# Kernel optimization log

Hardware: AMD Instinct MI355X
Metric: run time of the kernel (lower is better)

## Reference

```python
import jax, jax.numpy as jnp
import numpy as np

B, N, IN, H, DK, DV, OUT = 8, 1024, 512, 8, 64, 64, 512
SCALE = 1.0 / (DK ** 0.5)


def setup_inputs() -> dict:
    key = jax.random.key(0)
    ks = jax.random.split(key, 10)
    s = lambda fan_in: 1.0 / np.sqrt(fan_in)
    return {
        "x": jax.random.normal(ks[0], (B, N, IN), dtype=jnp.float32),
        "Wv": jax.random.uniform(ks[1], (IN, H * DV), jnp.float32, -s(IN), s(IN)),
        "bv": jax.random.uniform(ks[2], (H * DV,), jnp.float32, -s(IN), s(IN)),
        "Wk": jax.random.uniform(ks[3], (IN, H * DK), jnp.float32, -s(IN), s(IN)),
        "bk": jax.random.uniform(ks[4], (H * DK,), jnp.float32, -s(IN), s(IN)),
        "Wq": jax.random.uniform(ks[5], (IN, H * DK), jnp.float32, -s(IN), s(IN)),
        "bq": jax.random.uniform(ks[6], (H * DK,), jnp.float32, -s(IN), s(IN)),
        "Wo": jax.random.uniform(ks[7], (H * DV, OUT), jnp.float32, -s(H * DV), s(H * DV)),
        "bo": jax.random.uniform(ks[8], (OUT,), jnp.float32, -s(H * DV), s(H * DV)),
        "mask": jax.random.randint(ks[9], (B, N, N), 0, 2, dtype=jnp.int32),
    }


def reference(x, Wv, bv, Wk, bk, Wq, bq, Wo, bo, mask):
    # projections -> (B, N, H, d), vkq activation = relu
    v = jax.nn.relu((x @ Wv + bv).reshape(B, N, H, DV))
    q = jax.nn.relu((x @ Wq + bq).reshape(B, N, H, DK))
    k = jax.nn.relu((x @ Wk + bk).reshape(B, N, H, DK))
    # (B, H, N, d)
    q, k, v = (t.transpose(0, 2, 1, 3) for t in (q, k, v))
    # raw attention weights (returned pre-mask, pre-softmax): (B, H, N, N)
    att_weights = jnp.einsum("bhqd,bhkd->bhqk", q, k) * SCALE
    att = jnp.where(mask[:, None, :, :] == 0, -1e9, att_weights)
    att = jax.nn.softmax(att, axis=-1)
    out = jnp.einsum("bhqk,bhkd->bhqd", att, v) + v  # residual add of v
    out = out.transpose(0, 2, 1, 3).reshape(B, N, H * DV)
    out = jax.nn.relu(out @ Wo + bo)  # final activation = relu
    return out, att_weights
```

## Files before the change

kernel.cpp:

```cpp
#include <hip/hip_runtime.h>
#include <hip/hip_bf16.h>

typedef __attribute__((ext_vector_type(8))) short short8;
typedef __attribute__((ext_vector_type(4))) float f32x4;

#define DEV static __device__ __forceinline__

DEV unsigned short f2bf(float f) {
  union { float f; unsigned u; } v; v.f = f;
  unsigned r = v.u + 0x7FFFu + ((v.u >> 16) & 1u);
  return (unsigned short)(r >> 16);
}
DEV float bf2f(unsigned short b) {
  union { unsigned u; float f; } v; v.u = ((unsigned)b) << 16;
  return v.f;
}

DEV unsigned cvtpk_bf16(float lo, float hi) {
  unsigned r;
  asm("v_cvt_pk_bf16_f32 %0, %1, %2" : "=v"(r) : "v"(lo), "v"(hi));
  return r;
}

DEV void gld_lds16(const void* g, void* l) {
  __builtin_amdgcn_global_load_lds(
      (const __attribute__((address_space(1))) unsigned int*)g,
      (__attribute__((address_space(3))) unsigned int*)l, 16, 0, 0);
}

DEV short8 lds_read8(const unsigned short* base, int byteoff) {
  return *reinterpret_cast<const short8*>(reinterpret_cast<const char*>(base) + byteoff);
}

__global__ __launch_bounds__(256) void cast_x_kernel(const float* __restrict__ x,
                                                     unsigned short* __restrict__ xb, int n4) {
  int i = blockIdx.x * blockDim.x + threadIdx.x;
  if (i >= n4) return;
  float4 v = reinterpret_cast<const float4*>(x)[i];
  ushort4 o;
  o.x = f2bf(v.x); o.y = f2bf(v.y); o.z = f2bf(v.z); o.w = f2bf(v.w);
  reinterpret_cast<ushort4*>(xb)[i] = o;
}

__global__ __launch_bounds__(256) void mask_prep_kernel(const int* __restrict__ mask,
                                                        unsigned char* __restrict__ mb) {
  int i = blockIdx.x * 256 + threadIdx.x;
  int bq = i >> 8;
  int q = bq & 1023;
  int k = (i & 255) * 4;
  int4 m4 = reinterpret_cast<const int4*>(mask)[i];
  unsigned v = (m4.x ? 1u : 0u) | ((m4.y ? 1u : 0u) << 8) |
               ((m4.z ? 1u : 0u) << 16) | ((m4.w ? 1u : 0u) << 24);
  *reinterpret_cast<unsigned*>(mb + (size_t)bq * 1024 + (k ^ ((q & 7) << 2))) = v;
}

__global__ __launch_bounds__(256) void transpose_w_kernel(
    const float* __restrict__ W0, const float* __restrict__ W1,
    const float* __restrict__ W2, const float* __restrict__ W3,
    unsigned short* __restrict__ T0, unsigned short* __restrict__ T1,
    unsigned short* __restrict__ T2, unsigned short* __restrict__ T3) {
  const float* W = blockIdx.z == 0 ? W0 : blockIdx.z == 1 ? W1 : blockIdx.z == 2 ? W2 : W3;
  unsigned short* T = blockIdx.z == 0 ? T0 : blockIdx.z == 1 ? T1 : blockIdx.z == 2 ? T2 : T3;
  __shared__ unsigned short tile[32][33];
  int tx = threadIdx.x & 31, ty = threadIdx.x >> 5;
  int n0 = blockIdx.x * 32, k0 = blockIdx.y * 32;
#pragma unroll
  for (int i = 0; i < 32; i += 8)
    tile[ty + i][tx] = f2bf(W[(size_t)(k0 + ty + i) * 512 + n0 + tx]);
  __syncthreads();
#pragma unroll
  for (int i = 0; i < 32; i += 8)
    T[(size_t)(n0 + ty + i) * 512 + k0 + tx] = tile[tx][ty + i];
}

__global__ __launch_bounds__(256) void gemm_proj_kernel(
    const unsigned short* __restrict__ xb,
    const unsigned short* __restrict__ WqT, const unsigned short* __restrict__ WkT,
    const unsigned short* __restrict__ WvT,
    const float* __restrict__ bq, const float* __restrict__ bk, const float* __restrict__ bv,
    unsigned short* __restrict__ qn, unsigned short* __restrict__ kn,
    unsigned short* __restrict__ vn, unsigned short* __restrict__ vT) {
  const int z = blockIdx.z;
  const unsigned short* Wt = z == 0 ? WqT : z == 1 ? WkT : WvT;
  const float* bias = z == 0 ? bq : z == 1 ? bk : bv;
  unsigned short* outp = z == 0 ? qn : z == 1 ? kn : vn;

  __shared__ unsigned short smem[17408];
  unsigned short* As = smem;
  unsigned short* Bs = smem + 4096;

  const int tid = threadIdx.x;
  const int lane = tid & 63;
  const int w = tid >> 6;
  const int wm = w >> 1, wn = w & 1;
  const int lr = lane & 15;
  const int g = lane >> 4;

  const int m0 = blockIdx.x * 128;
  const int n0 = blockIdx.y * 128;

  f32x4 acc[4][4];
#pragma unroll
  for (int i = 0; i < 4; ++i)
#pragma unroll
    for (int j = 0; j < 4; ++j) acc[i][j] = (f32x4){0.f, 0.f, 0.f, 0.f};

  for (int kt = 0; kt < 16; ++kt) {
    const int k0 = kt * 32;
    __syncthreads();
#pragma unroll
    for (int p = 0; p < 2; ++p) {
      int slot = tid + 256 * p;
      int r = slot >> 2;
      int kg = (slot & 3) ^ ((r >> 1) & 3);
      unsigned short* ldsA = As + (size_t)((tid >> 6) + 4 * p) * 512;
      unsigned short* ldsB = Bs + (size_t)((tid >> 6) + 4 * p) * 512;
      gld_lds16(xb + (size_t)(m0 + r) * 512 + k0 + kg * 8, ldsA);
      gld_lds16(Wt + (size_t)(n0 + r) * 512 + k0 + kg * 8, ldsB);
    }
    __syncthreads();
    short8 af[4], bfr[4];
#pragma unroll
    for (int mi = 0; mi < 4; ++mi) {
      int r = wm * 64 + mi * 16 + lr;
      af[mi] = lds_read8(As, (r * 64 + g * 16) ^ (((r >> 1) & 3) << 4));
    }
#pragma unroll
    for (int ni = 0; ni < 4; ++ni) {
      int r = wn * 64 + ni * 16 + lr;
      bfr[ni] = lds_read8(Bs, (r * 64 + g * 16) ^ (((r >> 1) & 3) << 4));
    }
#pragma unroll
    for (int mi = 0; mi < 4; ++mi)
#pragma unroll
      for (int ni = 0; ni < 4; ++ni)
        acc[mi][ni] = __builtin_amdgcn_mfma_f32_16x16x32_bf16(af[mi], bfr[ni], acc[mi][ni], 0, 0, 0);
  }
  __syncthreads();

  float biasv[4];
#pragma unroll
  for (int ni = 0; ni < 4; ++ni) biasv[ni] = bias[n0 + wn * 64 + ni * 16 + lr];

#pragma unroll
  for (int mi = 0; mi < 4; ++mi) {
    int rowb = m0 + wm * 64 + mi * 16 + g * 4;
#pragma unroll
    for (int ni = 0; ni < 4; ++ni) {
      int c = n0 + wn * 64 + ni * 16 + lr;
      int h = c >> 6, d = c & 63;
#pragma unroll
      for (int rr = 0; rr < 4; ++rr) {
        float vf = acc[mi][ni][rr] + biasv[ni];
        vf = vf > 0.f ? vf : 0.f;
        unsigned short bvv = f2bf(vf);
        int row = rowb + rr;
        int b = row >> 10, tok = row & 1023;
        outp[((size_t)(b * 8 + h) * 1024 + tok) * 64 + d] = bvv;
        if (z == 2) {
          int cl = wn * 64 + ni * 16 + lr;
          int rl = wm * 64 + mi * 16 + g * 4 + rr;
          smem[cl * 136 + rl] = bvv;
        }
      }
    }
  }
  if (z == 2) {
    __syncthreads();
    int cl = tid >> 1, half = tid & 1;
    int gc = n0 + cl, h = gc >> 6, d = gc & 63;
    int b = m0 >> 10;
    int tokbase = (m0 & 1023) + half * 64;
    size_t base = (size_t)(b * 8 + h) * 65536 + (size_t)d * 1024 + tokbase;
    const unsigned short* src = smem + cl * 136 + half * 64;
#pragma unroll
    for (int j = 0; j < 8; ++j) {
      short8 v8 = *reinterpret_cast<const short8*>(src + j * 8);
      *reinterpret_cast<short8*>(vT + base + j * 8) = v8;
    }
  }
}

__global__ __launch_bounds__(256) void attn_kernel(
    const unsigned short* __restrict__ qg, const unsigned short* __restrict__ kgp,
    const unsigned short* __restrict__ vg, const unsigned short* __restrict__ vTg,
    const unsigned char* __restrict__ mb, float* __restrict__ attw,
    unsigned short* __restrict__ Og) {
  __shared__ unsigned short Ks[4096];
  __shared__ unsigned short Vs[4096];
  __shared__ unsigned char Mb[4096];
  __shared__ unsigned short Ps[4096];

  const int tid = threadIdx.x, lane = tid & 63, w = tid >> 6;
  const int lr = lane & 15, g = lane >> 4;
  const int bh = blockIdx.y, b = bh >> 3, h = bh & 7;
  const int q0 = blockIdx.x * 64;
  const int qw = q0 + w * 16;
  const size_t qbase = (size_t)bh * 65536;

  short8 aq[2];
#pragma unroll
  for (int dc = 0; dc < 2; ++dc)
    aq[dc] = *reinterpret_cast<const short8*>(qg + qbase + (size_t)(qw + lr) * 64 + dc * 32 + g * 8);

  f32x4 o[4];
#pragma unroll
  for (int di = 0; di < 4; ++di) o[di] = (f32x4){0.f, 0.f, 0.f, 0.f};
  float lsum = 0.f;

  unsigned short* Pw = Ps + w * 1024;
  const int gq = qw + lr;
  const int mrow = w * 16 + lr;

  for (int t = 0; t < 16; ++t) {
    const int kv0 = t * 64;
    __syncthreads();
#pragma unroll
    for (int p = 0; p < 2; ++p) {
      int slot = tid + 256 * p;
      int r = slot >> 3;
      int kgx = (slot & 7) ^ (r & 7);
      gld_lds16(kgp + qbase + (size_t)(kv0 + r) * 64 + kgx * 8,
                reinterpret_cast<char*>(Ks) + (w + 4 * p) * 1024);
      gld_lds16(vTg + qbase + (size_t)r * 1024 + kv0 + kgx * 8,
                reinterpret_cast<char*>(Vs) + (w + 4 * p) * 1024);
    }
    {
      int r = tid >> 2, seg = tid & 3;
      gld_lds16(mb + (size_t)(b * 1024 + q0 + r) * 1024 + kv0 + seg * 16,
                reinterpret_cast<char*>(Mb) + w * 1024);
    }
    __syncthreads();

    f32x4 s[4];
#pragma unroll
    for (int ni = 0; ni < 4; ++ni) s[ni] = (f32x4){0.f, 0.f, 0.f, 0.f};
#pragma unroll
    for (int ni = 0; ni < 4; ++ni) {
      int row = ni * 16 + lr;
#pragma unroll
      for (int dc = 0; dc < 2; ++dc) {
        short8 ak = lds_read8(Ks, (row * 128 + dc * 64 + g * 16) ^ ((row & 7) << 4));
        s[ni] = __builtin_amdgcn_mfma_f32_16x16x32_bf16(ak, aq[dc], s[ni], 0, 0, 0);
      }
    }

#pragma unroll
    for (int ni = 0; ni < 4; ++ni) {
      f32x4 sv = s[ni] * 0.125f;
      *reinterpret_cast<f32x4*>(attw + ((size_t)bh * 1024 + gq) * 1024 + kv0 + ni * 16 + g * 4) = sv;
      unsigned mk = *reinterpret_cast<const unsigned*>(
          Mb + ((mrow * 64 + ni * 16 + g * 4) ^ ((mrow & 7) << 2)));
      float p0 = (mk & 0x000000FFu) ? __expf(sv[0] - 16.f) : 0.f;
      float p1 = (mk & 0x0000FF00u) ? __expf(sv[1] - 16.f) : 0.f;
      float p2 = (mk & 0x00FF0000u) ? __expf(sv[2] - 16.f) : 0.f;
      float p3 = (mk & 0xFF000000u) ? __expf(sv[3] - 16.f) : 0.f;
      lsum += (p0 + p1) + (p2 + p3);
      uint2 pk = make_uint2(cvtpk_bf16(p0, p1), cvtpk_bf16(p2, p3));
      int pbyte = (lr * 128 + ni * 32 + g * 8) ^ ((lr & 7) << 4);
      *reinterpret_cast<uint2*>(reinterpret_cast<char*>(Pw) + pbyte) = pk;
    }

#pragma unroll
    for (int kc = 0; kc < 2; ++kc) {
      short8 ap = lds_read8(Pw, (lr * 128 + kc * 64 + g * 16) ^ ((lr & 7) << 4));
#pragma unroll
      for (int di = 0; di < 4; ++di) {
        int rd = di * 16 + lr;
        short8 bv8 = lds_read8(Vs, (rd * 128 + kc * 64 + g * 16) ^ ((rd & 7) << 4));
        o[di] = __builtin_amdgcn_mfma_f32_16x16x32_bf16(ap, bv8, o[di], 0, 0, 0);
      }
    }
  }

  float l = lsum;
  l += __shfl_xor(l, 16);
  l += __shfl_xor(l, 32);

#pragma unroll
  for (int rr = 0; rr < 4; ++rr) {
    int gq2 = qw + g * 4 + rr;
    float lq = __shfl(l, g * 4 + rr);
    float inv = 1.f / lq;
#pragma unroll
    for (int di = 0; di < 4; ++di) {
      int gd = di * 16 + lr;
      float ov = o[di][rr] * inv + bf2f(vg[qbase + (size_t)gq2 * 64 + gd]);
      Og[((size_t)(b * 1024 + gq2)) * 512 + h * 64 + gd] = f2bf(ov);
    }
  }
}

__global__ __launch_bounds__(256) void gemm_out_kernel(
    const unsigned short* __restrict__ Ab, const unsigned short* __restrict__ WoT,
    const float* __restrict__ bo, float* __restrict__ outp) {
  __shared__ unsigned short smem[8192];
  unsigned short* As = smem;
  unsigned short* Bs = smem + 4096;

  const int tid = threadIdx.x;
  const int lane = tid & 63;
  const int w = tid >> 6;
  const int wm = w >> 1, wn = w & 1;
  const int lr = lane & 15;
  const int g = lane >> 4;
  const int m0 = blockIdx.x * 128;
  const int n0 = blockIdx.y * 128;

  f32x4 acc[4][4];
#pragma unroll
  for (int i = 0; i < 4; ++i)
#pragma unroll
    for (int j = 0; j < 4; ++j) acc[i][j] = (f32x4){0.f, 0.f, 0.f, 0.f};

  for (int kt = 0; kt < 16; ++kt) {
    const int k0 = kt * 32;
    __syncthreads();
#pragma unroll
    for (int p = 0; p < 2; ++p) {
      int slot = tid + 256 * p;
      int r = slot >> 2;
      int kg = (slot & 3) ^ ((r >> 1) & 3);
      unsigned short* ldsA = As + (size_t)((tid >> 6) + 4 * p) * 512;
      unsigned short* ldsB = Bs + (size_t)((tid >> 6) + 4 * p) * 512;
      gld_lds16(Ab + (size_t)(m0 + r) * 512 + k0 + kg * 8, ldsA);
      gld_lds16(WoT + (size_t)(n0 + r) * 512 + k0 + kg * 8, ldsB);
    }
    __syncthreads();
    short8 af[4], bfr[4];
#pragma unroll
    for (int mi = 0; mi < 4; ++mi) {
      int r = wm * 64 + mi * 16 + lr;
      af[mi] = lds_read8(As, (r * 64 + g * 16) ^ (((r >> 1) & 3) << 4));
    }
#pragma unroll
    for (int ni = 0; ni < 4; ++ni) {
      int r = wn * 64 + ni * 16 + lr;
      bfr[ni] = lds_read8(Bs, (r * 64 + g * 16) ^ (((r >> 1) & 3) << 4));
    }
#pragma unroll
    for (int mi = 0; mi < 4; ++mi)
#pragma unroll
      for (int ni = 0; ni < 4; ++ni)
        acc[mi][ni] = __builtin_amdgcn_mfma_f32_16x16x32_bf16(af[mi], bfr[ni], acc[mi][ni], 0, 0, 0);
  }

  float biasv[4];
#pragma unroll
  for (int ni = 0; ni < 4; ++ni) biasv[ni] = bo[n0 + wn * 64 + ni * 16 + lr];
#pragma unroll
  for (int mi = 0; mi < 4; ++mi) {
    int rowb = m0 + wm * 64 + mi * 16 + g * 4;
#pragma unroll
    for (int ni = 0; ni < 4; ++ni) {
      int c = n0 + wn * 64 + ni * 16 + lr;
#pragma unroll
      for (int rr = 0; rr < 4; ++rr) {
        float vf = acc[mi][ni][rr] + biasv[ni];
        outp[(size_t)(rowb + rr) * 512 + c] = vf > 0.f ? vf : 0.f;
      }
    }
  }
}

extern "C" void kernel_launch(void* const* d_in, const int* in_sizes, int n_in,
                              void* d_out, int out_size, void* d_ws, size_t ws_size,
                              hipStream_t stream) {
  const float* x = (const float*)d_in[0];
  const float* Wv = (const float*)d_in[1];
  const float* bv = (const float*)d_in[2];
  const float* Wk = (const float*)d_in[3];
  const float* bk = (const float*)d_in[4];
  const float* Wq = (const float*)d_in[5];
  const float* bq = (const float*)d_in[6];
  const float* Wo = (const float*)d_in[7];
  const float* bo = (const float*)d_in[8];
  const int* mask = (const int*)d_in[9];

  char* ws = (char*)d_ws;
  unsigned short* xb  = (unsigned short*)(ws);
  unsigned char*  mbb = (unsigned char*)(ws);
  unsigned short* WqT = (unsigned short*)(ws + 8388608);
  unsigned short* WkT = (unsigned short*)(ws + 8912896);
  unsigned short* WvT = (unsigned short*)(ws + 9437184);
  unsigned short* WoT = (unsigned short*)(ws + 9961472);
  unsigned short* qn  = (unsigned short*)(ws + 10485760);
  unsigned short* kn  = (unsigned short*)(ws + 18874368);
  unsigned short* vn  = (unsigned short*)(ws + 27262976);
  unsigned short* vT  = (unsigned short*)(ws + 35651584);
  unsigned short* Og  = (unsigned short*)(ws + 44040192);

  float* outp = (float*)d_out;
  float* attw = (float*)d_out + 4194304;

  cast_x_kernel<<<4096, 256, 0, stream>>>(x, xb, 1048576);

  dim3 tg(16, 16, 4);
  transpose_w_kernel<<<tg, 256, 0, stream>>>(Wq, Wk, Wv, Wo, WqT, WkT, WvT, WoT);

  dim3 gp(64, 4, 3);
  gemm_proj_kernel<<<gp, 256, 0, stream>>>(xb, WqT, WkT, WvT, bq, bk, bv, qn, kn, vn, vT);

  mask_prep_kernel<<<8192, 256, 0, stream>>>(mask, mbb);

  dim3 ga(16, 64);
  attn_kernel<<<ga, 256, 0, stream>>>(qn, kn, vn, vT, mbb, attw, Og);

  dim3 go(64, 4);
  gemm_out_kernel<<<go, 256, 0, stream>>>(Og, WoT, bo, outp);
}
```

Before: 153.1 us.

## Load K, V and mask tiles directly from global into registers in attention

The attention kernel no longer stages K, V^T and mask tiles through shared memory with block-wide barriers. Each wave now loads its MFMA operands and mask words straight from global memory into registers (L2/L1 shared across the 4 waves), and the mask prep kernel writes a plain unswizzled byte layout to match. This removes both __syncthreads per tile and the LDS traffic, but each wave issues its own redundant global loads of K and V and uses more registers.

```diff
diff --git a/kernel.cpp b/kernel.cpp
--- a/kernel.cpp
+++ b/kernel.cpp
@@ -45,13 +45,10 @@
 __global__ __launch_bounds__(256) void mask_prep_kernel(const int* __restrict__ mask,
                                                         unsigned char* __restrict__ mb) {
   int i = blockIdx.x * 256 + threadIdx.x;
-  int bq = i >> 8;
-  int q = bq & 1023;
-  int k = (i & 255) * 4;
   int4 m4 = reinterpret_cast<const int4*>(mask)[i];
   unsigned v = (m4.x ? 1u : 0u) | ((m4.y ? 1u : 0u) << 8) |
                ((m4.z ? 1u : 0u) << 16) | ((m4.w ? 1u : 0u) << 24);
-  *reinterpret_cast<unsigned*>(mb + (size_t)bq * 1024 + (k ^ ((q & 7) << 2))) = v;
+  reinterpret_cast<unsigned*>(mb)[i] = v;
 }
 
 __global__ __launch_bounds__(256) void transpose_w_kernel(
@@ -186,22 +183,19 @@
     const unsigned short* __restrict__ vg, const unsigned short* __restrict__ vTg,
     const unsigned char* __restrict__ mb, float* __restrict__ attw,
     unsigned short* __restrict__ Og) {
-  __shared__ unsigned short Ks[4096];
-  __shared__ unsigned short Vs[4096];
-  __shared__ unsigned char Mb[4096];
   __shared__ unsigned short Ps[4096];
 
   const int tid = threadIdx.x, lane = tid & 63, w = tid >> 6;
   const int lr = lane & 15, g = lane >> 4;
   const int bh = blockIdx.y, b = bh >> 3, h = bh & 7;
-  const int q0 = blockIdx.x * 64;
-  const int qw = q0 + w * 16;
+  const int qw = blockIdx.x * 64 + w * 16;
   const size_t qbase = (size_t)bh * 65536;
+  const int gq = qw + lr;
 
   short8 aq[2];
 #pragma unroll
   for (int dc = 0; dc < 2; ++dc)
-    aq[dc] = *reinterpret_cast<const short8*>(qg + qbase + (size_t)(qw + lr) * 64 + dc * 32 + g * 8);
+    aq[dc] = *reinterpret_cast<const short8*>(qg + qbase + (size_t)gq * 64 + dc * 32 + g * 8);
 
   f32x4 o[4];
 #pragma unroll
@@ -209,52 +203,49 @@
   float lsum = 0.f;
 
   unsigned short* Pw = Ps + w * 1024;
-  const int gq = qw + lr;
-  const int mrow = w * 16 + lr;
+  const unsigned short* kp = kgp + qbase + (size_t)lr * 64 + g * 8;
+  const unsigned short* vp = vTg + qbase + (size_t)lr * 1024 + g * 8;
+  const unsigned char* mp = mb + ((size_t)(b * 1024 + gq)) * 1024 + g * 4;
+  float* awp = attw + ((size_t)bh * 1024 + gq) * 1024 + g * 4;
 
   for (int t = 0; t < 16; ++t) {
     const int kv0 = t * 64;
-    __syncthreads();
-#pragma unroll
-    for (int p = 0; p < 2; ++p) {
-      int slot = tid + 256 * p;
-      int r = slot >> 3;
-      int kgx = (slot & 7) ^ (r & 7);
-      gld_lds16(kgp + qbase + (size_t)(kv0 + r) * 64 + kgx * 8,
-                reinterpret_cast<char*>(Ks) + (w + 4 * p) * 1024);
-      gld_lds16(vTg + qbase + (size_t)r * 1024 + kv0 + kgx * 8,
-                reinterpret_cast<char*>(Vs) + (w + 4 * p) * 1024);
-    }
-    {
-      int r = tid >> 2, seg = tid & 3;
-      gld_lds16(mb + (size_t)(b * 1024 + q0 + r) * 1024 + kv0 + seg * 16,
-                reinterpret_cast<char*>(Mb) + w * 1024);
-    }
-    __syncthreads();
+
+    short8 ak[4][2], vv[4][2];
+    unsigned mk[4];
+#pragma unroll
+    for (int ni = 0; ni < 4; ++ni)
+#pragma unroll
+      for (int dc = 0; dc < 2; ++dc)
+        ak[ni][dc] =
+            *reinterpret_cast<const short8*>(kp + (size_t)(kv0 + ni * 16) * 64 + dc * 32);
+#pragma unroll
+    for (int di = 0; di < 4; ++di)
+#pragma unroll
+      for (int kc = 0; kc < 2; ++kc)
+        vv[di][kc] =
+            *reinterpret_cast<const short8*>(vp + (size_t)(di * 16) * 1024 + kv0 + kc * 32);
+#pragma unroll
+    for (int ni = 0; ni < 4; ++ni)
+      mk[ni] = *reinterpret_cast<const unsigned*>(mp + kv0 + ni * 16);
 
     f32x4 s[4];
 #pragma unroll
-    for (int ni = 0; ni < 4; ++ni) s[ni] = (f32x4){0.f, 0.f, 0.f, 0.f};
-#pragma unroll
-    for (int ni = 0; ni < 4; ++ni) {
-      int row = ni * 16 + lr;
-#pragma unroll
-      for (int dc = 0; dc < 2; ++dc) {
-        short8 ak = lds_read8(Ks, (row * 128 + dc * 64 + g * 16) ^ ((row & 7) << 4));
-        s[ni] = __builtin_amdgcn_mfma_f32_16x16x32_bf16(ak, aq[dc], s[ni], 0, 0, 0);
-      }
+    for (int ni = 0; ni < 4; ++ni) {
+      s[ni] = (f32x4){0.f, 0.f, 0.f, 0.f};
+      s[ni] = __builtin_amdgcn_mfma_f32_16x16x32_bf16(ak[ni][0], aq[0], s[ni], 0, 0, 0);
+      s[ni] = __builtin_amdgcn_mfma_f32_16x16x32_bf16(ak[ni][1], aq[1], s[ni], 0, 0, 0);
     }
 
 #pragma unroll
     for (int ni = 0; ni < 4; ++ni) {
       f32x4 sv = s[ni] * 0.125f;
-      *reinterpret_cast<f32x4*>(attw + ((size_t)bh * 1024 + gq) * 1024 + kv0 + ni * 16 + g * 4) = sv;
-      unsigned mk = *reinterpret_cast<const unsigned*>(
-          Mb + ((mrow * 64 + ni * 16 + g * 4) ^ ((mrow & 7) << 2)));
-      float p0 = (mk & 0x000000FFu) ? __expf(sv[0] - 16.f) : 0.f;
-      float p1 = (mk & 0x0000FF00u) ? __expf(sv[1] - 16.f) : 0.f;
-      float p2 = (mk & 0x00FF0000u) ? __expf(sv[2] - 16.f) : 0.f;
-      float p3 = (mk & 0xFF000000u) ? __expf(sv[3] - 16.f) : 0.f;
+      *reinterpret_cast<f32x4*>(awp + kv0 + ni * 16) = sv;
+      unsigned m = mk[ni];
+      float p0 = (m & 0x000000FFu) ? __expf(sv[0] - 16.f) : 0.f;
+      float p1 = (m & 0x0000FF00u) ? __expf(sv[1] - 16.f) : 0.f;
+      float p2 = (m & 0x00FF0000u) ? __expf(sv[2] - 16.f) : 0.f;
+      float p3 = (m & 0xFF000000u) ? __expf(sv[3] - 16.f) : 0.f;
       lsum += (p0 + p1) + (p2 + p3);
       uint2 pk = make_uint2(cvtpk_bf16(p0, p1), cvtpk_bf16(p2, p3));
       int pbyte = (lr * 128 + ni * 32 + g * 8) ^ ((lr & 7) << 4);
@@ -265,11 +256,8 @@
     for (int kc = 0; kc < 2; ++kc) {
       short8 ap = lds_read8(Pw, (lr * 128 + kc * 64 + g * 16) ^ ((lr & 7) << 4));
 #pragma unroll
-      for (int di = 0; di < 4; ++di) {
-        int rd = di * 16 + lr;
-        short8 bv8 = lds_read8(Vs, (rd * 128 + kc * 64 + g * 16) ^ ((rd & 7) << 4));
-        o[di] = __builtin_amdgcn_mfma_f32_16x16x32_bf16(ap, bv8, o[di], 0, 0, 0);
-      }
+      for (int di = 0; di < 4; ++di)
+        o[di] = __builtin_amdgcn_mfma_f32_16x16x32_bf16(ap, vv[di][kc], o[di], 0, 0, 0);
     }
   }
 
```

Result: slower. 220.4 us (+43.9%).
